# Kernel tuning notes

Measured on AMD Instinct MI355X. Metric: run time of the kernel, lower is better.

The kernel has to match this reference:

```python
import jax, jax.numpy as jnp
import numpy as np

B, LA, LS, C, H = 4, 1536, 512, 256, 4
DK = C // H
NEG = -jnp.inf


def _pad(lengths, maxlen):
    # True where padded (idx >= length)
    return jnp.arange(maxlen)[None, :] >= lengths[:, None]


def build_mask(l_v, l_s, ilens, ylens):
    """Additive float mask [B, l_v+l_s, l_v+l_s] with 0 / -inf, matching
    generate_multi_modal_mask_new."""
    b = ilens.shape[0]
    i = jnp.arange(l_s)
    causal = jnp.where(i[:, None] >= i[None, :], 0.0, NEG)            # [l_s, l_s]
    tgt_pad = _pad(ylens, l_s)                                        # [b, l_s]
    mask_s_s = jnp.where(tgt_pad[:, None, :], NEG, causal[None])      # [b, l_s, l_s]
    src_row = jnp.where(_pad(ilens, l_v), NEG, 0.0)                   # [b, l_v]
    mask_v_v = jnp.broadcast_to(src_row[:, None, :], (b, l_v, l_v))
    mask_s_v = jnp.broadcast_to(src_row[:, None, :], (b, l_s, l_v))
    mask_v_s = jnp.full((b, l_v, l_s), NEG, dtype=jnp.float32)
    top = jnp.concatenate([mask_v_v, mask_v_s], axis=2)
    bot = jnp.concatenate([mask_s_v, mask_s_s], axis=2)
    return jnp.concatenate([top, bot], axis=1)


def setup_inputs() -> dict:
    key = jax.random.key(0)
    ks = jax.random.split(key, 12)
    scale = 1.0 / np.sqrt(C)
    return {
        "audio_encoder_out": jax.random.normal(ks[0], (B, LA, C), jnp.float32),
        "text_encoder_out": jax.random.normal(ks[1], (B, LS, C), jnp.float32),
        "speech_length": jax.random.randint(ks[2], (B,), 1, LA),
        "text_length": jax.random.randint(ks[3], (B,), 1, LS),
        "Wq": jax.random.normal(ks[4], (C, C), jnp.float32) * scale,
        "bq": jax.random.normal(ks[5], (C,), jnp.float32) * scale,
        "Wk": jax.random.normal(ks[6], (C, C), jnp.float32) * scale,
        "bk": jax.random.normal(ks[7], (C,), jnp.float32) * scale,
        "Wv": jax.random.normal(ks[8], (C, C), jnp.float32) * scale,
        "bv": jax.random.normal(ks[9], (C,), jnp.float32) * scale,
        "Wo": jax.random.normal(ks[10], (C, C), jnp.float32) * scale,
        "bo": jax.random.normal(ks[11], (C,), jnp.float32) * scale,
    }


def reference(audio_encoder_out, text_encoder_out, speech_length, text_length,
              Wq, bq, Wk, bk, Wv, bv, Wo, bo):
    b, l_a, c = audio_encoder_out.shape
    l_s = text_encoder_out.shape[1]
    x = jnp.concatenate([audio_encoder_out, text_encoder_out], axis=1)  # [B, L, C]
    L = l_a + l_s

    def heads(W, bias):
        return (x @ W.T + bias).reshape(b, L, H, DK).transpose(0, 2, 1, 3)  # [B,H,L,DK]

    q, k, v = heads(Wq, bq), heads(Wk, bk), heads(Wv, bv)
    scores = jnp.einsum("bhqd,bhkd->bhqk", q, k) / np.float32(np.sqrt(DK))

    amask = build_mask(l_a, l_s, speech_length, text_length)  # additive [B,L,L]
    # Faithful to torch: mask.eq(0) positions (additive-0) are filled with -inf,
    # then zeroed in attn (the module's inverted masking behavior).
    eq0 = (amask == 0.0)[:, None, :, :]                       # [B,1,L,L]
    scores = jnp.where(eq0, NEG, scores)
    attn = jax.nn.softmax(scores, axis=-1)
    attn = jnp.where(eq0, 0.0, attn)                          # (dropout = identity, eval)
    out = jnp.einsum("bhqk,bhkd->bhqd", attn, v)
    out = out.transpose(0, 2, 1, 3).reshape(b, L, H * DK)
    return out @ Wo.T + bo
```

## Files before the change

### kernel.cpp

```cpp
#include <hip/hip_runtime.h>
#include <hip/hip_bf16.h>
#include <math.h>

#define LA 1536
#define LS 512
#define LT 2048
#define CC 256
#define NH 4
#define DKH 64
#define NB 4
#define NT (LT / 64)
#define NTA (LA / 64)

typedef _Float16 f16;
typedef __attribute__((ext_vector_type(8))) _Float16 f16x8;
typedef __attribute__((ext_vector_type(4))) _Float16 f16x4;
typedef __attribute__((ext_vector_type(4))) float f32x4;

__device__ inline f16x8 cvt8(const float4 a, const float4 b) {
    f16x8 h;
    h[0] = (_Float16)a.x; h[1] = (_Float16)a.y; h[2] = (_Float16)a.z; h[3] = (_Float16)a.w;
    h[4] = (_Float16)b.x; h[5] = (_Float16)b.y; h[6] = (_Float16)b.z; h[7] = (_Float16)b.w;
    return h;
}

__global__ __launch_bounds__(256) void qkv_mfma(
    const float* __restrict__ audio, const float* __restrict__ text,
    const float* __restrict__ Wq, const float* __restrict__ bq,
    const float* __restrict__ Wk, const float* __restrict__ bk,
    const float* __restrict__ Wv, const float* __restrict__ bv,
    f16* __restrict__ Qh, f16* __restrict__ Kh, f16* __restrict__ Vth)
{
    __shared__ f16 smem[128 * 64 + 64 * 64];
    f16* As = smem;
    f16* Bs = smem + 128 * 64;

    const int tid = threadIdx.x;
    const int w = tid >> 6, l = tid & 63;
    const int g = l >> 4, r = l & 15;

    const int m0 = blockIdx.x * 128;
    const int n0 = blockIdx.y * 64;
    const int mat = n0 >> 8;
    const int ch0 = n0 & 255;

    const float* W    = (mat == 0) ? Wq : (mat == 1) ? Wk : Wv;
    const float* bias = (mat == 0) ? bq : (mat == 1) ? bk : bv;

    const int b  = m0 >> 11;
    const int l0 = m0 & 2047;

    f32x4 acc[2][4] = {};

    for (int k0 = 0; k0 < CC; k0 += 64) {
        #pragma unroll
        for (int m = 0; m < 4; ++m) {
            const int idx = m * 256 + tid;
            const int row = idx >> 3, c = idx & 7;
            const int lrow = l0 + row;
            const float* src = (lrow < LA)
                ? (audio + ((size_t)b * LA + lrow) * CC + k0 + c * 8)
                : (text  + ((size_t)b * LS + (lrow - LA)) * CC + k0 + c * 8);
            const float4 x0 = *(const float4*)src;
            const float4 x1 = *(const float4*)(src + 4);
            *(f16x8*)(As + row * 64 + ((c ^ (row & 7)) << 3)) = cvt8(x0, x1);
        }
        #pragma unroll
        for (int m = 0; m < 2; ++m) {
            const int idx = m * 256 + tid;
            const int row = idx >> 3, c = idx & 7;
            const float* src = W + (size_t)(ch0 + row) * CC + k0 + c * 8;
            const float4 x0 = *(const float4*)src;
            const float4 x1 = *(const float4*)(src + 4);
            *(f16x8*)(Bs + row * 64 + ((c ^ (row & 7)) << 3)) = cvt8(x0, x1);
        }
        __syncthreads();
        #pragma unroll
        for (int kc = 0; kc < 2; ++kc) {
            f16x8 af[2];
            #pragma unroll
            for (int i = 0; i < 2; ++i) {
                const int row = w * 32 + i * 16 + r;
                const int c = kc * 4 + g;
                af[i] = *(const f16x8*)(As + row * 64 + ((c ^ (row & 7)) << 3));
            }
            f16x8 bf[4];
            #pragma unroll
            for (int j = 0; j < 4; ++j) {
                const int row = j * 16 + r;
                const int c = kc * 4 + g;
                bf[j] = *(const f16x8*)(Bs + row * 64 + ((c ^ (row & 7)) << 3));
            }
            #pragma unroll
            for (int i = 0; i < 2; ++i)
                #pragma unroll
                for (int j = 0; j < 4; ++j)
                    acc[i][j] = __builtin_amdgcn_mfma_f32_16x16x32_f16(af[i], bf[j], acc[i][j], 0, 0, 0);
        }
        __syncthreads();
    }

    float bcol[4];
    #pragma unroll
    for (int j = 0; j < 4; ++j) bcol[j] = bias[ch0 + j * 16 + r];

    if (mat <= 1) {
        f16* Out = (mat == 0) ? Qh : Kh;
        #pragma unroll
        for (int i = 0; i < 2; ++i)
            #pragma unroll
            for (int e = 0; e < 4; ++e) {
                const int m = m0 + w * 32 + i * 16 + g * 4 + e;
                #pragma unroll
                for (int j = 0; j < 4; ++j)
                    Out[(size_t)m * CC + ch0 + j * 16 + r] = (_Float16)(acc[i][j][e] + bcol[j]);
            }
    } else {
        f16* Ts = smem;
        #pragma unroll
        for (int i = 0; i < 2; ++i)
            #pragma unroll
            for (int e = 0; e < 4; ++e) {
                const int ml = w * 32 + i * 16 + g * 4 + e;
                #pragma unroll
                for (int j = 0; j < 4; ++j)
                    Ts[(j * 16 + r) * 136 + ml] = (_Float16)(acc[i][j][e] + bcol[j]);
            }
        __syncthreads();
        const int b2 = m0 >> 11, l0m = m0 & 2047;
        #pragma unroll
        for (int u = 0; u < 4; ++u) {
            const int idx = u * 256 + tid;
            const int nl = idx >> 4, mc = idx & 15;
            const f16x8 vv = *(const f16x8*)(Ts + nl * 136 + mc * 8);
            const int nglob = ch0 + nl;
            const int hh = nglob >> 6, dd = nglob & 63;
            *(f16x8*)(Vth + ((size_t)((b2 * NH + hh) * DKH + dd)) * LT + l0m + mc * 8) = vv;
        }
    }
}

__global__ __launch_bounds__(512) void attn_f16(
    const f16* __restrict__ Q, const f16* __restrict__ K,
    const f16* __restrict__ Vt,
    const int* __restrict__ slen, const int* __restrict__ tlen,
    f16* __restrict__ AO)
{
    __shared__ f16 Ks[2][4096];
    __shared__ f16 Vts[2][4096];
    __shared__ f16 Ps[8][16 * 72];
    __shared__ float Oc[4][1024];
    __shared__ float ML[2][64][2];

    const int tid = threadIdx.x;
    const int w = tid >> 6, l = tid & 63;
    const int gid = w >> 2, wg = w & 3;
    const int g = l >> 4, r = l & 15;
    const int tg = tid & 255;

    const int q0 = blockIdx.x * 64;
    const int h  = blockIdx.y;
    const int b  = blockIdx.z;

    const int ilen = slen[b];
    const int kcap = LA + tlen[b];
    const int nskip = ilen >> 6;
    int ntskip = 0;
    if (q0 >= LA) {
        const int skipmax = min(q0 - 63, kcap - 64);
        const int d = skipmax - LA;
        ntskip = (d < 0) ? 0 : ((d >> 6) + 1);
    }
    const int nAudio = NTA - nskip;
    const int nProc  = nAudio + (NT - NTA) - ntskip;
    const int nIter  = (nProc + 1) >> 1;

    const int qrow = q0 + 16 * wg + r;

    f16x8 qf[2];
    #pragma unroll
    for (int ch = 0; ch < 2; ++ch) {
        f16x8 q8 = *(const f16x8*)(Q + ((size_t)(b * LT) + qrow) * CC + h * DKH + ch * 32 + g * 8);
        #pragma unroll
        for (int e = 0; e < 8; ++e) q8[e] = q8[e] * (_Float16)0.125f;
        qf[ch] = q8;
    }

    const int srow0 = tg >> 3, scc = tg & 7;
    const int srow1 = srow0 + 32;
    const int sdst0 = srow0 * 64 + ((scc ^ (srow0 & 7)) << 3);
    const int sdst1 = srow1 * 64 + ((scc ^ (srow1 & 7)) << 3);

    #define TILE_OF(p) ((p) < nAudio ? (nskip + (p)) : (NTA + ntskip + ((p) - nAudio)))

    {
        const int k0 = TILE_OF(gid) * 64;
        *(f16x8*)(Ks[gid] + sdst0)  = *(const f16x8*)(K  + ((size_t)(b * LT) + k0 + srow0) * CC + h * DKH + scc * 8);
        *(f16x8*)(Vts[gid] + sdst0) = *(const f16x8*)(Vt + ((size_t)((b * NH + h) * DKH) + srow0) * LT + k0 + scc * 8);
        *(f16x8*)(Ks[gid] + sdst1)  = *(const f16x8*)(K  + ((size_t)(b * LT) + k0 + srow1) * CC + h * DKH + scc * 8);
        *(f16x8*)(Vts[gid] + sdst1) = *(const f16x8*)(Vt + ((size_t)((b * NH + h) * DKH) + srow1) * LT + k0 + scc * 8);
    }

    float m_run = -1e30f, l_run = 0.0f;
    f32x4 o[4] = {};

    for (int i = 0; i < nIter; ++i) {
        __syncthreads();
        const int pcur = 2 * i + gid;
        const bool curV = pcur < nProc;
        const bool nxtV = (pcur + 2) < nProc;

        f16x8 kr0, vr0, kr1, vr1;
        if (nxtV) {
            const int kn = TILE_OF(pcur + 2) * 64;
            kr0 = *(const f16x8*)(K  + ((size_t)(b * LT) + kn + srow0) * CC + h * DKH + scc * 8);
            vr0 = *(const f16x8*)(Vt + ((size_t)((b * NH + h) * DKH) + srow0) * LT + kn + scc * 8);
            kr1 = *(const f16x8*)(K  + ((size_t)(b * LT) + kn + srow1) * CC + h * DKH + scc * 8);
            vr1 = *(const f16x8*)(Vt + ((size_t)((b * NH + h) * DKH) + srow1) * LT + kn + scc * 8);
        }

        if (curV) {
            const int kt = TILE_OF(pcur);
            const int k0 = kt * 64;

            f32x4 sacc[4] = {};
            #pragma unroll
            for (int s = 0; s < 4; ++s) {
                const int row = 16 * s + r;
                #pragma unroll
                for (int ch = 0; ch < 2; ++ch) {
                    const f16x8 a = *(const f16x8*)(Ks[gid] + row * 64 + ((((ch * 4 + g) ^ (row & 7)) & 7) << 3));
                    sacc[s] = __builtin_amdgcn_mfma_f32_16x16x32_f16(a, qf[ch], sacc[s], 0, 0, 0);
                }
            }

            const int mode = (kt < NTA) ? ((k0 >= ilen) ? 0 : 1)
                                        : ((q0 < LA) ? 0 : 2);
            float sv[16];
            if (mode == 0) {
                #pragma unroll
                for (int s = 0; s < 4; ++s)
                    #pragma unroll
                    for (int e = 0; e < 4; ++e) sv[s * 4 + e] = sacc[s][e];
            } else if (mode == 1) {
                #pragma unroll
                for (int s = 0; s < 4; ++s)
                    #pragma unroll
                    for (int e = 0; e < 4; ++e) {
                        const int kk = k0 + 16 * s + 4 * g + e;
                        sv[s * 4 + e] = (kk >= ilen) ? sacc[s][e] : -INFINITY;
                    }
            } else {
                #pragma unroll
                for (int s = 0; s < 4; ++s)
                    #pragma unroll
                    for (int e = 0; e < 4; ++e) {
                        const int kk = k0 + 16 * s + 4 * g + e;
                        sv[s * 4 + e] = (kk > qrow || kk >= kcap) ? sacc[s][e] : -INFINITY;
                    }
            }

            float mloc = -1e30f;
            #pragma unroll
            for (int u = 0; u < 16; ++u) mloc = fmaxf(mloc, sv[u]);
            mloc = fmaxf(mloc, __shfl_xor(mloc, 16));
            mloc = fmaxf(mloc, __shfl_xor(mloc, 32));
            const float m_new = fmaxf(m_run, mloc);

            float ssum = 0.0f;
            f16x4 ph[4];
            #pragma unroll
            for (int s = 0; s < 4; ++s)
                #pragma unroll
                for (int e = 0; e < 4; ++e) {
                    const float p = __expf(sv[s * 4 + e] - m_new);
                    ph[s][e] = (_Float16)p;
                    ssum += p;
                }
            ssum += __shfl_xor(ssum, 16);
            ssum += __shfl_xor(ssum, 32);
            const float sc = __expf(m_run - m_new);
            l_run = l_run * sc + ssum;
            m_run = m_new;

            #pragma unroll
            for (int s = 0; s < 4; ++s)
                *(f16x4*)(&Ps[w][0] + r * 72 + 16 * s + 4 * g) = ph[s];

            #pragma unroll
            for (int e = 0; e < 4; ++e) {
                const float scr = __shfl(sc, 4 * g + e);
                #pragma unroll
                for (int dsb = 0; dsb < 4; ++dsb) o[dsb][e] *= scr;
            }

            #pragma unroll
            for (int ch = 0; ch < 2; ++ch) {
                const f16x8 a = *(const f16x8*)(&Ps[w][0] + r * 72 + ch * 32 + g * 8);
                #pragma unroll
                for (int dsb = 0; dsb < 4; ++dsb) {
                    const int vrow = 16 * dsb + r;
                    const f16x8 bf = *(const f16x8*)(Vts[gid] + vrow * 64 + ((((ch * 4 + g) ^ (vrow & 7)) & 7) << 3));
                    o[dsb] = __builtin_amdgcn_mfma_f32_16x16x32_f16(a, bf, o[dsb], 0, 0, 0);
                }
            }
        }

        __syncthreads();
        if (nxtV) {
            *(f16x8*)(Ks[gid] + sdst0)  = kr0;
            *(f16x8*)(Vts[gid] + sdst0) = vr0;
            *(f16x8*)(Ks[gid] + sdst1)  = kr1;
            *(f16x8*)(Vts[gid] + sdst1) = vr1;
        }
    }

    if (g == 0) {
        ML[gid][16 * wg + r][0] = m_run;
        ML[gid][16 * wg + r][1] = l_run;
    }
    if (gid == 1) {
        #pragma unroll
        for (int dsb = 0; dsb < 4; ++dsb)
            *(f32x4*)&Oc[wg][dsb * 256 + (g * 16 + r) * 4] = o[dsb];
    }
    __syncthreads();

    if (gid == 0) {
        #pragma unroll
        for (int e = 0; e < 4; ++e) {
            const int qloc = 16 * wg + 4 * g + e;
            const float m0v = ML[0][qloc][0], l0v = ML[0][qloc][1];
            const float m1v = ML[1][qloc][0], l1v = ML[1][qloc][1];
            const float mt = fmaxf(m0v, m1v);
            const float c0 = __expf(m0v - mt);
            const float c1 = __expf(m1v - mt);
            const float inv = 1.0f / (l0v * c0 + l1v * c1);
            const int qq = q0 + qloc;
            #pragma unroll
            for (int dsb = 0; dsb < 4; ++dsb) {
                const float of = (o[dsb][e] * c0 + Oc[wg][dsb * 256 + (g * 16 + r) * 4 + e] * c1) * inv;
                AO[((size_t)(b * LT) + qq) * CC + h * DKH + 16 * dsb + r] = (_Float16)of;
            }
        }
    }
    #undef TILE_OF
}

__global__ __launch_bounds__(256) void out_mfma(
    const f16* __restrict__ X, const float* __restrict__ Wo,
    const float* __restrict__ bo, float* __restrict__ Out)
{
    __shared__ f16 As[128 * 64];
    __shared__ f16 Bs[64 * 64];

    const int tid = threadIdx.x;
    const int w = tid >> 6, l = tid & 63;
    const int g = l >> 4, r = l & 15;

    const int m0 = blockIdx.x * 128;
    const int n0 = blockIdx.y * 64;

    f32x4 acc[2][4] = {};

    for (int k0 = 0; k0 < CC; k0 += 64) {
        #pragma unroll
        for (int m = 0; m < 4; ++m) {
            const int idx = m * 256 + tid;
            const int row = idx >> 3, c = idx & 7;
            *(f16x8*)(As + row * 64 + ((c ^ (row & 7)) << 3)) =
                *(const f16x8*)(X + (size_t)(m0 + row) * CC + k0 + c * 8);
        }
        #pragma unroll
        for (int m = 0; m < 2; ++m) {
            const int idx = m * 256 + tid;
            const int row = idx >> 3, c = idx & 7;
            const float* src = Wo + (size_t)(n0 + row) * CC + k0 + c * 8;
            const float4 x0 = *(const float4*)src;
            const float4 x1 = *(const float4*)(src + 4);
            *(f16x8*)(Bs + row * 64 + ((c ^ (row & 7)) << 3)) = cvt8(x0, x1);
        }
        __syncthreads();
        #pragma unroll
        for (int kc = 0; kc < 2; ++kc) {
            f16x8 af[2];
            #pragma unroll
            for (int i = 0; i < 2; ++i) {
                const int row = w * 32 + i * 16 + r;
                const int c = kc * 4 + g;
                af[i] = *(const f16x8*)(As + row * 64 + ((c ^ (row & 7)) << 3));
            }
            f16x8 bf[4];
            #pragma unroll
            for (int j = 0; j < 4; ++j) {
                const int row = j * 16 + r;
                const int c = kc * 4 + g;
                bf[j] = *(const f16x8*)(Bs + row * 64 + ((c ^ (row & 7)) << 3));
            }
            #pragma unroll
            for (int i = 0; i < 2; ++i)
                #pragma unroll
                for (int j = 0; j < 4; ++j)
                    acc[i][j] = __builtin_amdgcn_mfma_f32_16x16x32_f16(af[i], bf[j], acc[i][j], 0, 0, 0);
        }
        __syncthreads();
    }

    float bcol[4];
    #pragma unroll
    for (int j = 0; j < 4; ++j) bcol[j] = bo[n0 + j * 16 + r];

    #pragma unroll
    for (int i = 0; i < 2; ++i)
        #pragma unroll
        for (int e = 0; e < 4; ++e) {
            const int m = m0 + w * 32 + i * 16 + g * 4 + e;
            #pragma unroll
            for (int j = 0; j < 4; ++j)
                Out[(size_t)m * CC + n0 + j * 16 + r] = acc[i][j][e] + bcol[j];
        }
}

extern "C" void kernel_launch(void* const* d_in, const int* in_sizes, int n_in,
                              void* d_out, int out_size, void* d_ws, size_t ws_size,
                              hipStream_t stream)
{
    const float* audio = (const float*)d_in[0];
    const float* text  = (const float*)d_in[1];
    const int*   slen  = (const int*)d_in[2];
    const int*   tlen  = (const int*)d_in[3];
    const float* Wq = (const float*)d_in[4];
    const float* bq = (const float*)d_in[5];
    const float* Wk = (const float*)d_in[6];
    const float* bk = (const float*)d_in[7];
    const float* Wv = (const float*)d_in[8];
    const float* bv = (const float*)d_in[9];
    const float* Wo = (const float*)d_in[10];
    const float* bo = (const float*)d_in[11];
    float* out = (float*)d_out;

    const size_t SZ = (size_t)NB * LT * CC;
    f16* Qh  = (f16*)d_ws;
    f16* Kh  = Qh + SZ;
    f16* Vth = Kh + SZ;
    f16* AOh = Vth + SZ;

    qkv_mfma<<<dim3(64, 12), 256, 0, stream>>>(audio, text, Wq, bq, Wk, bk, Wv, bv,
                                               Qh, Kh, Vth);
    attn_f16<<<dim3(LT / 64, NH, NB), 512, 0, stream>>>(Qh, Kh, Vth, slen, tlen, AOh);
    out_mfma<<<dim3(64, 4), 256, 0, stream>>>(AOh, Wo, bo, out);
}
```

Measured before the change: 49.30 us.

## Rewrite attention with 32x32 MFMA tiles, exp2 softmax and register-held P

The attention kernel moves from 16x16x32 to 32x32x16 MFMA, with each wave owning 32 query rows, and drops from 512 to 256 threads per block with a 4-blocks-per-CU launch bound. The 1/sqrt(dk)*log2(e) scale is folded into the Q projection so softmax can use exp2f. The probabilities stay in registers as the B operand, which removes the P shared-memory round trip and the rescale shuffles, and the output rescale is skipped when the running max is unchanged. K/V loading becomes a synchronous load-then-compute per tile, replacing the register prefetch. That gives up some latency hiding in exchange for less shared memory and higher occupancy.

```diff
diff --git a/kernel.cpp b/kernel.cpp
--- a/kernel.cpp
+++ b/kernel.cpp
@@ -11,11 +11,15 @@
 #define NB 4
 #define NT (LT / 64)
 #define NTA (LA / 64)
+#define SZ ((size_t)NB * LT * CC)
+
+#define QSCALE 0.1803368801111244f
 
 typedef _Float16 f16;
 typedef __attribute__((ext_vector_type(8))) _Float16 f16x8;
 typedef __attribute__((ext_vector_type(4))) _Float16 f16x4;
 typedef __attribute__((ext_vector_type(4))) float f32x4;
+typedef __attribute__((ext_vector_type(16))) float f32x16;
 
 __device__ inline f16x8 cvt8(const float4 a, const float4 b) {
     f16x8 h;
@@ -23,6 +27,8 @@
     h[4] = (_Float16)b.x; h[5] = (_Float16)b.y; h[6] = (_Float16)b.z; h[7] = (_Float16)b.w;
     return h;
 }
+
+#define SIG(j) (((j) & ~12) | (((j) & 4) << 1) | (((j) & 8) >> 1))
 
 __global__ __launch_bounds__(256) void qkv_mfma(
     const float* __restrict__ audio, const float* __restrict__ text,
@@ -106,6 +112,7 @@
 
     if (mat <= 1) {
         f16* Out = (mat == 0) ? Qh : Kh;
+        const float osc = (mat == 0) ? QSCALE : 1.0f;
         #pragma unroll
         for (int i = 0; i < 2; ++i)
             #pragma unroll
@@ -113,7 +120,8 @@
                 const int m = m0 + w * 32 + i * 16 + g * 4 + e;
                 #pragma unroll
                 for (int j = 0; j < 4; ++j)
-                    Out[(size_t)m * CC + ch0 + j * 16 + r] = (_Float16)(acc[i][j][e] + bcol[j]);
+                    Out[(size_t)m * CC + ch0 + j * 16 + r] =
+                        (_Float16)((acc[i][j][e] + bcol[j]) * osc);
             }
     } else {
         f16* Ts = smem;
@@ -140,23 +148,19 @@
     }
 }
 
-__global__ __launch_bounds__(512) void attn_f16(
+__global__ __launch_bounds__(256, 4) void attn_f16(
     const f16* __restrict__ Q, const f16* __restrict__ K,
     const f16* __restrict__ Vt,
     const int* __restrict__ slen, const int* __restrict__ tlen,
     f16* __restrict__ AO)
 {
-    __shared__ f16 Ks[2][4096];
-    __shared__ f16 Vts[2][4096];
-    __shared__ f16 Ps[8][16 * 72];
-    __shared__ float Oc[4][1024];
-    __shared__ float ML[2][64][2];
+    __shared__ __align__(16) f16 Ks[2][4096];
+    __shared__ __align__(16) f16 Vts[2][4096];
 
     const int tid = threadIdx.x;
     const int w = tid >> 6, l = tid & 63;
-    const int gid = w >> 2, wg = w & 3;
-    const int g = l >> 4, r = l & 15;
-    const int tg = tid & 255;
+    const int gid = w >> 1, qh = w & 1;
+    const int lo = l & 31, hi = l >> 5;
 
     const int q0 = blockIdx.x * 64;
     const int h  = blockIdx.y;
@@ -175,174 +179,172 @@
     const int nProc  = nAudio + (NT - NTA) - ntskip;
     const int nIter  = (nProc + 1) >> 1;
 
-    const int qrow = q0 + 16 * wg + r;
-
-    f16x8 qf[2];
+    const int qrow = q0 + 32 * qh + lo;
+
+    f16x8 qf[4];
     #pragma unroll
-    for (int ch = 0; ch < 2; ++ch) {
-        f16x8 q8 = *(const f16x8*)(Q + ((size_t)(b * LT) + qrow) * CC + h * DKH + ch * 32 + g * 8);
-        #pragma unroll
-        for (int e = 0; e < 8; ++e) q8[e] = q8[e] * (_Float16)0.125f;
-        qf[ch] = q8;
-    }
-
-    const int srow0 = tg >> 3, scc = tg & 7;
-    const int srow1 = srow0 + 32;
-    const int sdst0 = srow0 * 64 + ((scc ^ (srow0 & 7)) << 3);
-    const int sdst1 = srow1 * 64 + ((scc ^ (srow1 & 7)) << 3);
+    for (int c = 0; c < 4; ++c)
+        qf[c] = *(const f16x8*)(Q + ((size_t)(b * LT) + qrow) * CC + h * DKH + 16 * c + 8 * hi);
+
+    const int srw = l >> 3, scc = l & 7;
 
     #define TILE_OF(p) ((p) < nAudio ? (nskip + (p)) : (NTA + ntskip + ((p) - nAudio)))
 
-    {
-        const int k0 = TILE_OF(gid) * 64;
-        *(f16x8*)(Ks[gid] + sdst0)  = *(const f16x8*)(K  + ((size_t)(b * LT) + k0 + srow0) * CC + h * DKH + scc * 8);
-        *(f16x8*)(Vts[gid] + sdst0) = *(const f16x8*)(Vt + ((size_t)((b * NH + h) * DKH) + srow0) * LT + k0 + scc * 8);
-        *(f16x8*)(Ks[gid] + sdst1)  = *(const f16x8*)(K  + ((size_t)(b * LT) + k0 + srow1) * CC + h * DKH + scc * 8);
-        *(f16x8*)(Vts[gid] + sdst1) = *(const f16x8*)(Vt + ((size_t)((b * NH + h) * DKH) + srow1) * LT + k0 + scc * 8);
-    }
-
     float m_run = -1e30f, l_run = 0.0f;
-    f32x4 o[4] = {};
+    f32x16 o[2] = {};
 
     for (int i = 0; i < nIter; ++i) {
-        __syncthreads();
         const int pcur = 2 * i + gid;
         const bool curV = pcur < nProc;
-        const bool nxtV = (pcur + 2) < nProc;
-
-        f16x8 kr0, vr0, kr1, vr1;
-        if (nxtV) {
-            const int kn = TILE_OF(pcur + 2) * 64;
-            kr0 = *(const f16x8*)(K  + ((size_t)(b * LT) + kn + srow0) * CC + h * DKH + scc * 8);
-            vr0 = *(const f16x8*)(Vt + ((size_t)((b * NH + h) * DKH) + srow0) * LT + kn + scc * 8);
-            kr1 = *(const f16x8*)(K  + ((size_t)(b * LT) + kn + srow1) * CC + h * DKH + scc * 8);
-            vr1 = *(const f16x8*)(Vt + ((size_t)((b * NH + h) * DKH) + srow1) * LT + kn + scc * 8);
-        }
+
+        __syncthreads();
+        if (curV) {
+            const int k0 = TILE_OF(pcur) * 64;
+            f16x8 kreg[4], vreg[4];
+            #pragma unroll
+            for (int t = 0; t < 4; ++t) {
+                const int sr = 8 * (4 * qh + t) + srw;
+                kreg[t] = *(const f16x8*)(K + ((size_t)(b * LT) + k0 + sr) * CC + h * DKH + scc * 8);
+                vreg[t] = *(const f16x8*)(Vt + ((size_t)((b * NH + h) * DKH) + sr) * LT + k0 + scc * 8);
+            }
+            #pragma unroll
+            for (int t = 0; t < 4; ++t) {
+                const int sr = 8 * (4 * qh + t) + srw;
+                const int kr = SIG(sr);
+                *(f16x8*)(Ks[gid] + kr * 64 + ((scc ^ (kr & 7)) << 3)) = kreg[t];
+                *(f16x8*)(Vts[gid] + sr * 64 + ((scc ^ (sr & 7)) << 3)) = vreg[t];
+            }
+        }
+        __syncthreads();
 
         if (curV) {
             const int kt = TILE_OF(pcur);
             const int k0 = kt * 64;
-
-            f32x4 sacc[4] = {};
-            #pragma unroll
-            for (int s = 0; s < 4; ++s) {
-                const int row = 16 * s + r;
-                #pragma unroll
-                for (int ch = 0; ch < 2; ++ch) {
-                    const f16x8 a = *(const f16x8*)(Ks[gid] + row * 64 + ((((ch * 4 + g) ^ (row & 7)) & 7) << 3));
-                    sacc[s] = __builtin_amdgcn_mfma_f32_16x16x32_f16(a, qf[ch], sacc[s], 0, 0, 0);
-                }
+            const f16* Kb = Ks[gid];
+            const f16* Vb = Vts[gid];
+
+            f32x16 s0 = {}, s1 = {};
+            #pragma unroll
+            for (int c = 0; c < 4; ++c) {
+                const int cc = 2 * c + hi;
+                const int r0 = lo;
+                const f16x8 a0 = *(const f16x8*)(Kb + r0 * 64 + ((cc ^ (r0 & 7)) << 3));
+                s0 = __builtin_amdgcn_mfma_f32_32x32x16_f16(a0, qf[c], s0, 0, 0, 0);
+                const int r1 = 32 + lo;
+                const f16x8 a1 = *(const f16x8*)(Kb + r1 * 64 + ((cc ^ (r1 & 7)) << 3));
+                s1 = __builtin_amdgcn_mfma_f32_32x32x16_f16(a1, qf[c], s1, 0, 0, 0);
             }
 
             const int mode = (kt < NTA) ? ((k0 >= ilen) ? 0 : 1)
                                         : ((q0 < LA) ? 0 : 2);
-            float sv[16];
-            if (mode == 0) {
-                #pragma unroll
-                for (int s = 0; s < 4; ++s)
-                    #pragma unroll
-                    for (int e = 0; e < 4; ++e) sv[s * 4 + e] = sacc[s][e];
-            } else if (mode == 1) {
-                #pragma unroll
-                for (int s = 0; s < 4; ++s)
-                    #pragma unroll
-                    for (int e = 0; e < 4; ++e) {
-                        const int kk = k0 + 16 * s + 4 * g + e;
-                        sv[s * 4 + e] = (kk >= ilen) ? sacc[s][e] : -INFINITY;
-                    }
-            } else {
-                #pragma unroll
-                for (int s = 0; s < 4; ++s)
-                    #pragma unroll
-                    for (int e = 0; e < 4; ++e) {
-                        const int kk = k0 + 16 * s + 4 * g + e;
-                        sv[s * 4 + e] = (kk > qrow || kk >= kcap) ? sacc[s][e] : -INFINITY;
-                    }
+            if (mode == 1) {
+                #pragma unroll
+                for (int reg = 0; reg < 16; ++reg) {
+                    const int kk0 = k0 + 16 * ((reg >> 3) & 1) + 8 * hi + 4 * ((reg >> 2) & 1) + (reg & 3);
+                    if (kk0 < ilen)      s0[reg] = -INFINITY;
+                    if (kk0 + 32 < ilen) s1[reg] = -INFINITY;
+                }
+            } else if (mode == 2) {
+                #pragma unroll
+                for (int reg = 0; reg < 16; ++reg) {
+                    const int kk0 = k0 + 16 * ((reg >> 3) & 1) + 8 * hi + 4 * ((reg >> 2) & 1) + (reg & 3);
+                    if (!(kk0 > qrow || kk0 >= kcap))           s0[reg] = -INFINITY;
+                    const int kk1 = kk0 + 32;
+                    if (!(kk1 > qrow || kk1 >= kcap))           s1[reg] = -INFINITY;
+                }
             }
 
             float mloc = -1e30f;
             #pragma unroll
-            for (int u = 0; u < 16; ++u) mloc = fmaxf(mloc, sv[u]);
-            mloc = fmaxf(mloc, __shfl_xor(mloc, 16));
+            for (int reg = 0; reg < 16; ++reg) {
+                mloc = fmaxf(mloc, s0[reg]);
+                mloc = fmaxf(mloc, s1[reg]);
+            }
             mloc = fmaxf(mloc, __shfl_xor(mloc, 32));
             const float m_new = fmaxf(m_run, mloc);
 
             float ssum = 0.0f;
-            f16x4 ph[4];
-            #pragma unroll
-            for (int s = 0; s < 4; ++s)
-                #pragma unroll
-                for (int e = 0; e < 4; ++e) {
-                    const float p = __expf(sv[s * 4 + e] - m_new);
-                    ph[s][e] = (_Float16)p;
+            f16x8 pb[4];
+            #pragma unroll
+            for (int kp = 0; kp < 4; ++kp)
+                #pragma unroll
+                for (int e = 0; e < 8; ++e) {
+                    const int reg = 8 * (kp & 1) + 4 * (e >> 2) + (e & 3);
+                    const float sval = (kp < 2) ? s0[reg] : s1[reg];
+                    const float p = exp2f(sval - m_new);
+                    pb[kp][e] = (_Float16)p;
                     ssum += p;
                 }
-            ssum += __shfl_xor(ssum, 16);
             ssum += __shfl_xor(ssum, 32);
-            const float sc = __expf(m_run - m_new);
-            l_run = l_run * sc + ssum;
-            m_run = m_new;
-
-            #pragma unroll
-            for (int s = 0; s < 4; ++s)
-                *(f16x4*)(&Ps[w][0] + r * 72 + 16 * s + 4 * g) = ph[s];
-
-            #pragma unroll
-            for (int e = 0; e < 4; ++e) {
-                const float scr = __shfl(sc, 4 * g + e);
-                #pragma unroll
-                for (int dsb = 0; dsb < 4; ++dsb) o[dsb][e] *= scr;
-            }
-
-            #pragma unroll
-            for (int ch = 0; ch < 2; ++ch) {
-                const f16x8 a = *(const f16x8*)(&Ps[w][0] + r * 72 + ch * 32 + g * 8);
-                #pragma unroll
-                for (int dsb = 0; dsb < 4; ++dsb) {
-                    const int vrow = 16 * dsb + r;
-                    const f16x8 bf = *(const f16x8*)(Vts[gid] + vrow * 64 + ((((ch * 4 + g) ^ (vrow & 7)) & 7) << 3));
-                    o[dsb] = __builtin_amdgcn_mfma_f32_16x16x32_f16(a, bf, o[dsb], 0, 0, 0);
+
+            if (__all(m_new == m_run)) {
+                l_run += ssum;
+            } else {
+                const float sc = exp2f(m_run - m_new);
+                l_run = l_run * sc + ssum;
+                m_run = m_new;
+                #pragma unroll
+                for (int dh = 0; dh < 2; ++dh)
+                    #pragma unroll
+                    for (int reg = 0; reg < 16; ++reg)
+                        o[dh][reg] *= sc;
+            }
+
+            #pragma unroll
+            for (int kp = 0; kp < 4; ++kp) {
+                const int cc = 2 * kp + hi;
+                #pragma unroll
+                for (int dh = 0; dh < 2; ++dh) {
+                    const int dr = 32 * dh + lo;
+                    const f16x8 a = *(const f16x8*)(Vb + dr * 64 + ((cc ^ (dr & 7)) << 3));
+                    o[dh] = __builtin_amdgcn_mfma_f32_32x32x16_f16(a, pb[kp], o[dh], 0, 0, 0);
                 }
             }
         }
-
-        __syncthreads();
-        if (nxtV) {
-            *(f16x8*)(Ks[gid] + sdst0)  = kr0;
-            *(f16x8*)(Vts[gid] + sdst0) = vr0;
-            *(f16x8*)(Ks[gid] + sdst1)  = kr1;
-            *(f16x8*)(Vts[gid] + sdst1) = vr1;
-        }
-    }
-
-    if (g == 0) {
-        ML[gid][16 * wg + r][0] = m_run;
-        ML[gid][16 * wg + r][1] = l_run;
-    }
+    }
+
+    float* OcF = (float*)&Ks[0][0];
+    float* ML1 = (float*)&Vts[0][0];
+    __syncthreads();
     if (gid == 1) {
         #pragma unroll
-        for (int dsb = 0; dsb < 4; ++dsb)
-            *(f32x4*)&Oc[wg][dsb * 256 + (g * 16 + r) * 4] = o[dsb];
+        for (int dh = 0; dh < 2; ++dh)
+            #pragma unroll
+            for (int u4 = 0; u4 < 4; ++u4) {
+                f32x4 v;
+                #pragma unroll
+                for (int v2 = 0; v2 < 4; ++v2) v[v2] = o[dh][4 * u4 + v2];
+                *(f32x4*)(OcF + (((qh * 2 + dh) << 10) + (l << 4) + 4 * u4)) = v;
+            }
+        if (hi == 0) {
+            ML1[(qh * 32 + lo) * 2 + 0] = m_run;
+            ML1[(qh * 32 + lo) * 2 + 1] = l_run;
+        }
     }
     __syncthreads();
 
     if (gid == 0) {
-        #pragma unroll
-        for (int e = 0; e < 4; ++e) {
-            const int qloc = 16 * wg + 4 * g + e;
-            const float m0v = ML[0][qloc][0], l0v = ML[0][qloc][1];
-            const float m1v = ML[1][qloc][0], l1v = ML[1][qloc][1];
-            const float mt = fmaxf(m0v, m1v);
-            const float c0 = __expf(m0v - mt);
-            const float c1 = __expf(m1v - mt);
-            const float inv = 1.0f / (l0v * c0 + l1v * c1);
-            const int qq = q0 + qloc;
-            #pragma unroll
-            for (int dsb = 0; dsb < 4; ++dsb) {
-                const float of = (o[dsb][e] * c0 + Oc[wg][dsb * 256 + (g * 16 + r) * 4 + e] * c1) * inv;
-                AO[((size_t)(b * LT) + qq) * CC + h * DKH + 16 * dsb + r] = (_Float16)of;
-            }
-        }
+        const float m1 = ML1[(qh * 32 + lo) * 2 + 0];
+        const float l1 = ML1[(qh * 32 + lo) * 2 + 1];
+        const float mt = fmaxf(m_run, m1);
+        const float c0 = exp2f(m_run - mt);
+        const float c1 = exp2f(m1 - mt);
+        const float inv = 1.0f / (l_run * c0 + l1 * c1);
+        #pragma unroll
+        for (int dh = 0; dh < 2; ++dh)
+            #pragma unroll
+            for (int u4 = 0; u4 < 4; ++u4) {
+                f16x4 outv;
+                #pragma unroll
+                for (int v2 = 0; v2 < 4; ++v2) {
+                    const int reg = 4 * u4 + v2;
+                    const float val = (o[dh][reg] * c0
+                                     + OcF[((qh * 2 + dh) << 10) + (l << 4) + reg] * c1) * inv;
+                    outv[v2] = (_Float16)val;
+                }
+                *(f16x4*)(AO + ((size_t)(b * LT) + qrow) * CC + h * DKH
+                          + 32 * dh + 8 * u4 + 4 * hi) = outv;
+            }
     }
     #undef TILE_OF
 }
@@ -439,7 +441,6 @@
     const float* bo = (const float*)d_in[11];
     float* out = (float*)d_out;
 
-    const size_t SZ = (size_t)NB * LT * CC;
     f16* Qh  = (f16*)d_ws;
     f16* Kh  = Qh + SZ;
     f16* Vth = Kh + SZ;
@@ -447,6 +448,6 @@
 
     qkv_mfma<<<dim3(64, 12), 256, 0, stream>>>(audio, text, Wq, bq, Wk, bk, Wv, bv,
                                                Qh, Kh, Vth);
-    attn_f16<<<dim3(LT / 64, NH, NB), 512, 0, stream>>>(Qh, Kh, Vth, slen, tlen, AOh);
+    attn_f16<<<dim3(LT / 64, NH, NB), 256, 0, stream>>>(Qh, Kh, Vth, slen, tlen, AOh);
     out_mfma<<<dim3(64, 4), 256, 0, stream>>>(AOh, Wo, bo, out);
 }
```

New measurement: 60.45 us. 1.23x slower.
